# Kernel tuning notes

Hardware: AMD Instinct MI355X
Metric: run time of the kernel (lower is better)

## Reference

```python
import jax, jax.numpy as jnp
import numpy as np

B, S, H, NH = 4, 2048, 1024, 16
HD = H // NH
EPS = 1e-12


def setup_inputs() -> dict:
    key = jax.random.key(0)
    ks = jax.random.split(key, 12)
    sc = 0.02
    return {
        "query": jax.random.normal(ks[0], (B, S, H), dtype=jnp.float32),
        "attention_mask": jnp.zeros((B, 1, 1, S), dtype=jnp.float32),
        "Wq": jax.random.normal(ks[1], (H, H), dtype=jnp.float32) * sc,
        "bq": jnp.zeros((H,), dtype=jnp.float32),
        "Wk": jax.random.normal(ks[2], (H, H), dtype=jnp.float32) * sc,
        "bk": jnp.zeros((H,), dtype=jnp.float32),
        "Wv": jax.random.normal(ks[3], (H, H), dtype=jnp.float32) * sc,
        "bv": jnp.zeros((H,), dtype=jnp.float32),
        "Wd": jax.random.normal(ks[4], (H, H), dtype=jnp.float32) * sc,
        "bd": jnp.zeros((H,), dtype=jnp.float32),
        "ln_gamma": jnp.ones((H,), dtype=jnp.float32),
        "ln_beta": jnp.zeros((H,), dtype=jnp.float32),
    }


def reference(query, attention_mask, Wq, bq, Wk, bk, Wv, bv, Wd, bd, ln_gamma, ln_beta):
    # QKV projections: [B,S,H] -> [B,S,NH,HD]
    q = (query @ Wq + bq).reshape(B, S, NH, HD)
    k = (query @ Wk + bk).reshape(B, S, NH, HD)
    v = (query @ Wv + bv).reshape(B, S, NH, HD)
    # scores: [B,NH,S,S]
    scores = jnp.einsum("bqhd,bkhd->bhqk", q, k) / jnp.sqrt(jnp.float32(HD))
    scores = scores + attention_mask
    probs = jax.nn.softmax(scores, axis=-1)  # attn_dropout p=0 (eval)
    ctx = jnp.einsum("bhqk,bkhd->bqhd", probs, v).reshape(B, S, H)
    hidden = ctx @ Wd + bd  # out_dropout p=0 (eval)
    # pre-LN residual path: LN(hidden) + query
    mu = jnp.mean(hidden, axis=-1, keepdims=True)
    var = jnp.mean(jnp.square(hidden - mu), axis=-1, keepdims=True)
    hidden = (hidden - mu) * jax.lax.rsqrt(var + EPS) * ln_gamma + ln_beta
    return hidden + query
```

## Files before the change

### kernel.cpp

```cpp
#include <hip/hip_runtime.h>
#include <stdint.h>

#define Bn 4
#define Sn 2048
#define Hn 1024
#define NHn 16
#define Mn 8192

typedef unsigned short bf_t;
typedef __attribute__((ext_vector_type(8))) short s16x8;
typedef __attribute__((ext_vector_type(4))) short s16x4;
typedef __attribute__((ext_vector_type(8))) unsigned short u16x8;
typedef __attribute__((ext_vector_type(4))) unsigned short u16x4;
typedef __attribute__((ext_vector_type(4))) float f32x4;
typedef __attribute__((ext_vector_type(4))) unsigned int u32x4;
typedef __attribute__((ext_vector_type(2))) unsigned int u32x2;

__device__ __forceinline__ bf_t f2bf(float f) {
  unsigned int u = __float_as_uint(f);
  u += 0x7fffu + ((u >> 16) & 1u);
  return (bf_t)(u >> 16);
}

__device__ __forceinline__ unsigned pk2(float lo, float hi) {
  return __builtin_amdgcn_perm(__float_as_uint(hi), __float_as_uint(lo), 0x07060302u);
}
__device__ __forceinline__ s16x4 pack4(float a0, float a1, float a2, float a3) {
  u32x2 t;
  t[0] = pk2(a0, a1);
  t[1] = pk2(a2, a3);
  return __builtin_bit_cast(s16x4, t);
}

#define MFMA16K16(a, b, c) __builtin_amdgcn_mfma_f32_16x16x16bf16_1k(a, b, c, 0, 0, 0)

#define GLOAD16(gp, lp) __builtin_amdgcn_global_load_lds(              \
    (__attribute__((address_space(1))) void*)(gp),                     \
    (__attribute__((address_space(3))) void*)(lp), 16, 0, 0)

__global__ __launch_bounds__(256)
void cvt_bf16(const float* __restrict__ x, bf_t* __restrict__ y) {
  size_t i = ((size_t)blockIdx.x * 256 + threadIdx.x) * 4;
  const f32x4 v = *(const f32x4*)(x + i);
  u16x4 o;
  o[0] = f2bf(v[0]); o[1] = f2bf(v[1]); o[2] = f2bf(v[2]); o[3] = f2bf(v[3]);
  *(u16x4*)(y + i) = o;
}

__global__ __launch_bounds__(256)
void wtrans4(const float* __restrict__ Wq, const float* __restrict__ Wk,
             const float* __restrict__ Wv, const float* __restrict__ Wd,
             bf_t* __restrict__ Wt, bf_t* __restrict__ Wdt) {
  __shared__ float tile[32][33];
  const int z = blockIdx.z;
  const float* W = (z == 0) ? Wq : (z == 1) ? Wk : (z == 2) ? Wv : Wd;
  bf_t* dst = (z < 3) ? Wt + (size_t)z * Hn * Hn : Wdt;
  const int tx = threadIdx.x;
  const int ty = threadIdx.y;
  const int n0 = blockIdx.x * 32, k0 = blockIdx.y * 32;
#pragma unroll
  for (int i = 0; i < 4; i++)
    tile[ty + i * 8][tx] = W[(size_t)(k0 + ty + i * 8) * Hn + n0 + tx];
  __syncthreads();
#pragma unroll
  for (int i = 0; i < 4; i++) {
    const int nn = ty + i * 8, kk = tx;
    dst[(size_t)(n0 + nn) * Hn + k0 + kk] = f2bf(tile[kk][nn]);
  }
}

__global__ __launch_bounds__(256, 3)
void gemm_bt(const bf_t* __restrict__ A, const bf_t* __restrict__ Bt,
             const float* __restrict__ b0, const float* __restrict__ b1,
             const float* __restrict__ b2, void* __restrict__ outp,
             int N, int K, int out_bf16)
{
  __shared__ bf_t As[2][4096];
  __shared__ bf_t Bs[2][4096];
  const int tid = threadIdx.x;
  const int wave = tid >> 6, lane = tid & 63;
  const int l15 = lane & 15, quad = lane >> 4;
  const int bm = blockIdx.y * 128, bn = blockIdx.x * 128;
  const int wm = (wave >> 1) * 64, wn = (wave & 1) * 64;
  const int srow = tid >> 2;
  const int scol = (tid & 3) * 8;

  const bf_t* Ag = A + (size_t)(bm + srow) * K + scol;
  const bf_t* Bg = Bt + (size_t)(bn + srow) * K + scol;

  f32x4 acc[4][4] = {};

  GLOAD16(Ag, As[0] + tid * 8);
  GLOAD16(Ag + (size_t)64 * K, As[0] + 2048 + tid * 8);
  GLOAD16(Bg, Bs[0] + tid * 8);
  GLOAD16(Bg + (size_t)64 * K, Bs[0] + 2048 + tid * 8);

  const int nIter = K >> 5;
  for (int i = 0; i < nIter; i++) {
    const int cur = i & 1;
    __syncthreads();
    if (i + 1 < nIter) {
      const int k0 = (i + 1) * 32;
      GLOAD16(Ag + k0, As[cur ^ 1] + tid * 8);
      GLOAD16(Ag + (size_t)64 * K + k0, As[cur ^ 1] + 2048 + tid * 8);
      GLOAD16(Bg + k0, Bs[cur ^ 1] + tid * 8);
      GLOAD16(Bg + (size_t)64 * K + k0, Bs[cur ^ 1] + 2048 + tid * 8);
    }
    s16x8 af[4], bfr[4];
#pragma unroll
    for (int mi = 0; mi < 4; mi++)
      af[mi] = *(const s16x8*)&As[cur][(wm + mi * 16 + l15) * 32 + quad * 8];
#pragma unroll
    for (int ni = 0; ni < 4; ni++)
      bfr[ni] = *(const s16x8*)&Bs[cur][(wn + ni * 16 + l15) * 32 + quad * 8];
#pragma unroll
    for (int mi = 0; mi < 4; mi++)
#pragma unroll
      for (int ni = 0; ni < 4; ni++)
        acc[mi][ni] = __builtin_amdgcn_mfma_f32_16x16x32_bf16(af[mi], bfr[ni], acc[mi][ni], 0, 0, 0);
  }

#pragma unroll
  for (int ni = 0; ni < 4; ni++) {
    const int gn = bn + wn + ni * 16 + l15;
    const float* bp = (gn < 1024) ? b0 : ((gn < 2048) ? b1 : b2);
    const float bias = bp[gn & 1023];
#pragma unroll
    for (int mi = 0; mi < 4; mi++) {
#pragma unroll
      for (int r = 0; r < 4; r++) {
        const int gm = bm + wm + mi * 16 + quad * 4 + r;
        const float v = acc[mi][ni][r] + bias;
        if (out_bf16) ((bf_t*)outp)[(size_t)gm * N + gn] = f2bf(v);
        else          ((float*)outp)[(size_t)gm * N + gn] = v;
      }
    }
  }
}

__global__ __launch_bounds__(256)
void kvswz(const bf_t* __restrict__ qkv, bf_t* __restrict__ Kf,
           bf_t* __restrict__ Vf, const float* __restrict__ mask,
           float* __restrict__ mask2) {
  __shared__ u32x4 smbuf[640];
  const int t = threadIdx.x;
  const int bh = blockIdx.y, b = bh >> 4, h = bh & 15;
  const int k0 = blockIdx.x * 64;

  if (blockIdx.z == 0) {
    bf_t* KT = (bf_t*)smbuf;
#pragma unroll
    for (int i = 0; i < 2; i++) {
      const int c = t + i * 256;
      const int row = c >> 3, col8 = (c & 7) * 8;
      const u16x8 v = *(const u16x8*)(qkv + (size_t)(b * Sn + k0 + row) * 3072 + 1024 + h * 64 + col8);
      *(u16x8*)&KT[row * 80 + col8] = v;
    }
    __syncthreads();
    bf_t* dst0 = Kf + ((size_t)(bh * 32 + blockIdx.x) * 8) * 512;
#pragma unroll
    for (int i = 0; i < 2; i++) {
      const int p = t + i * 256;
      const int frag = p >> 6, lane = p & 63;
      const int ks = frag >> 1, half = frag & 1;
      const int l15 = lane & 15, quad = lane >> 4;
      const u16x8 v = *(const u16x8*)&KT[(ks * 16 + l15) * 80 + half * 32 + quad * 8];
      *(u16x8*)(dst0 + (size_t)frag * 512 + lane * 8) = v;
    }
  } else {
    unsigned int* P32 = (unsigned int*)smbuf;
    {
      const int kp = t >> 3;
      const int d0 = (t & 7) * 8;
      const bf_t* p0 = qkv + (size_t)(b * Sn + k0 + 2 * kp) * 3072 + 2048 + h * 64 + d0;
      const u16x8 r0 = *(const u16x8*)p0;
      const u16x8 r1 = *(const u16x8*)(p0 + 3072);
#pragma unroll
      for (int j = 0; j < 8; j++)
        P32[(d0 + j) * 33 + kp] = (unsigned)r0[j] | ((unsigned)r1[j] << 16);
    }
    if (h == 0 && t < 64)
      mask2[b * Sn + k0 + t] = mask[b * Sn + k0 + t] * 1.44269504f;
    __syncthreads();
    bf_t* dst0 = Vf + ((size_t)(bh * 32 + blockIdx.x) * 8) * 512;
#pragma unroll
    for (int i = 0; i < 2; i++) {
      const int p = t + i * 256;
      const int fp = p >> 6, lane = p & 63;
      const int dvblk = fp >> 1, kpair = fp & 1;
      const int l15 = lane & 15, quad = (lane >> 4) & 3;
      const int d = dvblk * 16 + l15;
      const int c = kpair * 16 + quad * 2;
      u32x4 w;
      w[0] = P32[d * 33 + c];
      w[1] = P32[d * 33 + c + 1];
      w[2] = P32[d * 33 + c + 8];
      w[3] = P32[d * 33 + c + 9];
      *(u32x4*)(dst0 + (size_t)fp * 512 + lane * 8) = w;
    }
  }
}

__global__ __launch_bounds__(256)
void attn(const bf_t* __restrict__ qkv, const bf_t* __restrict__ Kf,
          const bf_t* __restrict__ Vf, const float* __restrict__ mask2,
          bf_t* __restrict__ ctx)
{
  __shared__ bf_t Ks[2][4096];
  __shared__ bf_t Vs[2][4096];

  const int tid = threadIdx.x;
  const int wave = tid >> 6, lane = tid & 63;
  const int l15 = lane & 15, quad = lane >> 4;
  const int idx = blockIdx.x;
  const int bh = idx & 63, b = bh >> 4, h = bh & 15;
  const int q0 = (idx >> 6) * 128;

  s16x8 aq[2][2];
#pragma unroll
  for (int qf = 0; qf < 2; qf++) {
    const bf_t* qp = qkv + (size_t)(b * Sn + q0 + wave * 32 + qf * 16 + l15) * 3072 + h * 64;
    aq[qf][0] = *(const s16x8*)(qp + quad * 8);
    aq[qf][1] = *(const s16x8*)(qp + 32 + quad * 8);
  }

  f32x4 lacc[2] = {};
  f32x4 o[2][4] = {};
  const s16x4 ONES = {16256, 16256, 16256, 16256};

  const bf_t* kb = Kf + (size_t)bh * 32 * 4096;
  const bf_t* vb = Vf + (size_t)bh * 32 * 4096;
  const float* m2row = mask2 + (size_t)b * Sn;

  const float C1 = 0.125f * 1.44269504f;

#pragma unroll
  for (int c = 0; c < 2; c++) {
    GLOAD16(kb + c * 2048 + tid * 8, Ks[0] + c * 2048 + tid * 8);
    GLOAD16(vb + c * 2048 + tid * 8, Vs[0] + c * 2048 + tid * 8);
  }

  for (int it = 0; it < 32; ++it) {
    const int cur = it & 1;
    __syncthreads();
    if (it < 31) {
      const bf_t* kn = kb + (size_t)(it + 1) * 4096;
      const bf_t* vn = vb + (size_t)(it + 1) * 4096;
#pragma unroll
      for (int c = 0; c < 2; c++) {
        GLOAD16(kn + c * 2048 + tid * 8, Ks[cur ^ 1] + c * 2048 + tid * 8);
        GLOAD16(vn + c * 2048 + tid * 8, Vs[cur ^ 1] + c * 2048 + tid * 8);
      }
    }

    s16x4 pb[2][4];
#pragma unroll
    for (int e = 0; e < 4; e++) {
      const s16x8 k0f = *(const s16x8*)&Ks[cur][(e * 2 + 0) * 512 + lane * 8];
      const s16x8 k1f = *(const s16x8*)&Ks[cur][(e * 2 + 1) * 512 + lane * 8];
      const f32x4 mk2 = *(const f32x4*)(m2row + it * 64 + e * 16 + quad * 4);
#pragma unroll
      for (int qf = 0; qf < 2; qf++) {
        f32x4 acc = {};
        acc = __builtin_amdgcn_mfma_f32_16x16x32_bf16(k0f, aq[qf][0], acc, 0, 0, 0);
        acc = __builtin_amdgcn_mfma_f32_16x16x32_bf16(k1f, aq[qf][1], acc, 0, 0, 0);
        const float p0 = __builtin_exp2f(fmaf(acc[0], C1, mk2[0]));
        const float p1 = __builtin_exp2f(fmaf(acc[1], C1, mk2[1]));
        const float p2 = __builtin_exp2f(fmaf(acc[2], C1, mk2[2]));
        const float p3 = __builtin_exp2f(fmaf(acc[3], C1, mk2[3]));
        pb[qf][e] = pack4(p0, p1, p2, p3);
        lacc[qf] = MFMA16K16(ONES, pb[qf][e], lacc[qf]);
      }
    }

#pragma unroll
    for (int kpair = 0; kpair < 2; kpair++)
#pragma unroll
      for (int dvblk = 0; dvblk < 4; dvblk++) {
        const s16x8 vv = *(const s16x8*)&Vs[cur][(dvblk * 2 + kpair) * 512 + lane * 8];
        const s16x4 vlo = {vv[0], vv[1], vv[2], vv[3]};
        const s16x4 vhi = {vv[4], vv[5], vv[6], vv[7]};
#pragma unroll
        for (int qf = 0; qf < 2; qf++) {
          o[qf][dvblk] = MFMA16K16(vlo, pb[qf][kpair * 2 + 0], o[qf][dvblk]);
          o[qf][dvblk] = MFMA16K16(vhi, pb[qf][kpair * 2 + 1], o[qf][dvblk]);
        }
      }
  }

#pragma unroll
  for (int qf = 0; qf < 2; qf++) {
    const float inv = 1.f / lacc[qf][0];
    const size_t row = (size_t)(b * Sn + q0 + wave * 32 + qf * 16 + l15);
#pragma unroll
    for (int dvblk = 0; dvblk < 4; dvblk++) {
      u16x4 ov;
#pragma unroll
      for (int r = 0; r < 4; r++) ov[r] = f2bf(o[qf][dvblk][r] * inv);
      *(u16x4*)&ctx[row * Hn + h * 64 + dvblk * 16 + quad * 4] = ov;
    }
  }
}

__global__ __launch_bounds__(256)
void ln_res(const float* __restrict__ hid, const float* __restrict__ query,
            const float* __restrict__ gamma, const float* __restrict__ beta,
            float* __restrict__ out)
{
  const int row = blockIdx.x, t = threadIdx.x;
  const f32x4 h = *(const f32x4*)(hid + (size_t)row * Hn + t * 4);
  float s = h[0] + h[1] + h[2] + h[3];
  float ss = h[0]*h[0] + h[1]*h[1] + h[2]*h[2] + h[3]*h[3];
#pragma unroll
  for (int m = 32; m; m >>= 1) { s += __shfl_xor(s, m); ss += __shfl_xor(ss, m); }
  __shared__ float red[8];
  if ((t & 63) == 0) { red[t >> 6] = s; red[4 + (t >> 6)] = ss; }
  __syncthreads();
  s = red[0] + red[1] + red[2] + red[3];
  ss = red[4] + red[5] + red[6] + red[7];
  const float mu = s * (1.f / Hn);
  const float rs = rsqrtf(ss * (1.f / Hn) - mu * mu + 1e-12f);
  const f32x4 q = *(const f32x4*)(query + (size_t)row * Hn + t * 4);
  const f32x4 g = *(const f32x4*)(gamma + t * 4);
  const f32x4 be = *(const f32x4*)(beta + t * 4);
  f32x4 o;
#pragma unroll
  for (int j = 0; j < 4; j++) o[j] = (h[j] - mu) * rs * g[j] + be[j] + q[j];
  *(f32x4*)(out + (size_t)row * Hn + t * 4) = o;
}

extern "C" void kernel_launch(void* const* d_in, const int* in_sizes, int n_in,
                              void* d_out, int out_size, void* d_ws, size_t ws_size,
                              hipStream_t stream) {
  const float* query = (const float*)d_in[0];
  const float* mask  = (const float*)d_in[1];
  const float* Wq = (const float*)d_in[2];
  const float* bq = (const float*)d_in[3];
  const float* Wk = (const float*)d_in[4];
  const float* bk = (const float*)d_in[5];
  const float* Wv = (const float*)d_in[6];
  const float* bv = (const float*)d_in[7];
  const float* Wd = (const float*)d_in[8];
  const float* bd = (const float*)d_in[9];
  const float* gamma = (const float*)d_in[10];
  const float* beta  = (const float*)d_in[11];

  char* w = (char*)d_ws;
  bf_t* Xb  = (bf_t*)w;  w += (size_t)Mn * Hn * 2;
  bf_t* Wt  = (bf_t*)w;  w += (size_t)3 * Hn * Hn * 2;
  bf_t* Wdt = (bf_t*)w;  w += (size_t)Hn * Hn * 2;
  bf_t* QKV = (bf_t*)w;  w += (size_t)Mn * 3 * Hn * 2;
  bf_t* Vf  = (bf_t*)w;  w += (size_t)64 * 32 * 4096 * 2;
  bf_t* Ctx = (bf_t*)w;  w += (size_t)Mn * Hn * 2;
  bf_t* Kf  = (bf_t*)w;
  float* Hid = (float*)w;  w += (size_t)Mn * Hn * 4;
  float* Mask2 = (float*)w;

  cvt_bf16<<<Mn * Hn / 1024, 256, 0, stream>>>(query, Xb);
  wtrans4<<<dim3(32, 32, 4), dim3(32, 8), 0, stream>>>(Wq, Wk, Wv, Wd, Wt, Wdt);
  gemm_bt<<<dim3(24, 64), 256, 0, stream>>>(Xb, Wt, bq, bk, bv, QKV, 3072, 1024, 1);
  kvswz<<<dim3(32, 64, 2), 256, 0, stream>>>(QKV, Kf, Vf, mask, Mask2);
  attn<<<1024, 256, 0, stream>>>(QKV, Kf, Vf, Mask2, Ctx);
  gemm_bt<<<dim3(8, 64), 256, 0, stream>>>(Ctx, Wdt, bd, bd, bd, Hid, 1024, 1024, 0);
  ln_res<<<Mn, 256, 0, stream>>>(Hid, query, gamma, beta, (float*)d_out);
}
```

Baseline: 362.7 us.

## Merge prep kernels, stage mask in LDS, use native exp2 in attention

Combines the query-to-bf16 conversion and the weight transposes into one launch by adding a fifth z-slice that converts the query, which removes one kernel launch. The attention kernel now copies the 2048-entry mask row into shared memory once per block instead of reading it from global memory on every iteration. It also swaps exp2f for the native amdgcn exp2 intrinsic, which drops the range handling. The mask staging adds 8 KB of LDS per block, which may lower occupancy.

```diff
diff --git a/kernel.cpp b/kernel.cpp
--- a/kernel.cpp
+++ b/kernel.cpp
@@ -39,24 +39,29 @@
     (__attribute__((address_space(3))) void*)(lp), 16, 0, 0)
 
 __global__ __launch_bounds__(256)
-void cvt_bf16(const float* __restrict__ x, bf_t* __restrict__ y) {
-  size_t i = ((size_t)blockIdx.x * 256 + threadIdx.x) * 4;
-  const f32x4 v = *(const f32x4*)(x + i);
-  u16x4 o;
-  o[0] = f2bf(v[0]); o[1] = f2bf(v[1]); o[2] = f2bf(v[2]); o[3] = f2bf(v[3]);
-  *(u16x4*)(y + i) = o;
-}
-
-__global__ __launch_bounds__(256)
-void wtrans4(const float* __restrict__ Wq, const float* __restrict__ Wk,
-             const float* __restrict__ Wv, const float* __restrict__ Wd,
-             bf_t* __restrict__ Wt, bf_t* __restrict__ Wdt) {
+void prep(const float* __restrict__ Wq, const float* __restrict__ Wk,
+          const float* __restrict__ Wv, const float* __restrict__ Wd,
+          const float* __restrict__ query,
+          bf_t* __restrict__ Wt, bf_t* __restrict__ Wdt, bf_t* __restrict__ Xb) {
   __shared__ float tile[32][33];
   const int z = blockIdx.z;
+  const int tx = threadIdx.x;
+  const int ty = threadIdx.y;
+  if (z == 4) {
+    const int bid = blockIdx.y * 32 + blockIdx.x;
+    const int t = ty * 32 + tx;
+    const size_t base = (size_t)bid * 8192 + t * 4;
+#pragma unroll
+    for (int i = 0; i < 8; i++) {
+      const f32x4 v = *(const f32x4*)(query + base + i * 1024);
+      u16x4 o;
+      o[0] = f2bf(v[0]); o[1] = f2bf(v[1]); o[2] = f2bf(v[2]); o[3] = f2bf(v[3]);
+      *(u16x4*)(Xb + base + i * 1024) = o;
+    }
+    return;
+  }
   const float* W = (z == 0) ? Wq : (z == 1) ? Wk : (z == 2) ? Wv : Wd;
   bf_t* dst = (z < 3) ? Wt + (size_t)z * Hn * Hn : Wdt;
-  const int tx = threadIdx.x;
-  const int ty = threadIdx.y;
   const int n0 = blockIdx.x * 32, k0 = blockIdx.y * 32;
 #pragma unroll
   for (int i = 0; i < 4; i++)
@@ -208,6 +213,7 @@
 {
   __shared__ bf_t Ks[2][4096];
   __shared__ bf_t Vs[2][4096];
+  __shared__ float Ms[2048];
 
   const int tid = threadIdx.x;
   const int wave = tid >> 6, lane = tid & 63;
@@ -216,6 +222,14 @@
   const int bh = idx & 63, b = bh >> 4, h = bh & 15;
   const int q0 = (idx >> 6) * 128;
 
+  {
+    const float* m2row = mask2 + (size_t)b * Sn;
+    const f32x4 m0 = *(const f32x4*)(m2row + tid * 8);
+    const f32x4 m1 = *(const f32x4*)(m2row + tid * 8 + 4);
+    *(f32x4*)&Ms[tid * 8] = m0;
+    *(f32x4*)&Ms[tid * 8 + 4] = m1;
+  }
+
   s16x8 aq[2][2];
 #pragma unroll
   for (int qf = 0; qf < 2; qf++) {
@@ -230,7 +244,6 @@
 
   const bf_t* kb = Kf + (size_t)bh * 32 * 4096;
   const bf_t* vb = Vf + (size_t)bh * 32 * 4096;
-  const float* m2row = mask2 + (size_t)b * Sn;
 
   const float C1 = 0.125f * 1.44269504f;
 
@@ -258,16 +271,16 @@
     for (int e = 0; e < 4; e++) {
       const s16x8 k0f = *(const s16x8*)&Ks[cur][(e * 2 + 0) * 512 + lane * 8];
       const s16x8 k1f = *(const s16x8*)&Ks[cur][(e * 2 + 1) * 512 + lane * 8];
-      const f32x4 mk2 = *(const f32x4*)(m2row + it * 64 + e * 16 + quad * 4);
+      const f32x4 mk2 = *(const f32x4*)&Ms[it * 64 + e * 16 + quad * 4];
 #pragma unroll
       for (int qf = 0; qf < 2; qf++) {
         f32x4 acc = {};
         acc = __builtin_amdgcn_mfma_f32_16x16x32_bf16(k0f, aq[qf][0], acc, 0, 0, 0);
         acc = __builtin_amdgcn_mfma_f32_16x16x32_bf16(k1f, aq[qf][1], acc, 0, 0, 0);
-        const float p0 = __builtin_exp2f(fmaf(acc[0], C1, mk2[0]));
-        const float p1 = __builtin_exp2f(fmaf(acc[1], C1, mk2[1]));
-        const float p2 = __builtin_exp2f(fmaf(acc[2], C1, mk2[2]));
-        const float p3 = __builtin_exp2f(fmaf(acc[3], C1, mk2[3]));
+        const float p0 = __builtin_amdgcn_exp2f(fmaf(acc[0], C1, mk2[0]));
+        const float p1 = __builtin_amdgcn_exp2f(fmaf(acc[1], C1, mk2[1]));
+        const float p2 = __builtin_amdgcn_exp2f(fmaf(acc[2], C1, mk2[2]));
+        const float p3 = __builtin_amdgcn_exp2f(fmaf(acc[3], C1, mk2[3]));
         pb[qf][e] = pack4(p0, p1, p2, p3);
         lacc[qf] = MFMA16K16(ONES, pb[qf][e], lacc[qf]);
       }
@@ -356,8 +369,7 @@
   float* Hid = (float*)w;  w += (size_t)Mn * Hn * 4;
   float* Mask2 = (float*)w;
 
-  cvt_bf16<<<Mn * Hn / 1024, 256, 0, stream>>>(query, Xb);
-  wtrans4<<<dim3(32, 32, 4), dim3(32, 8), 0, stream>>>(Wq, Wk, Wv, Wd, Wt, Wdt);
+  prep<<<dim3(32, 32, 5), dim3(32, 8), 0, stream>>>(Wq, Wk, Wv, Wd, query, Wt, Wdt, Xb);
   gemm_bt<<<dim3(24, 64), 256, 0, stream>>>(Xb, Wt, bq, bk, bv, QKV, 3072, 1024, 1);
   kvswz<<<dim3(32, 64, 2), 256, 0, stream>>>(QKV, Kf, Vf, mask, Mask2);
   attn<<<1024, 256, 0, stream>>>(QKV, Kf, Vf, Mask2, Ctx);
```

Measured after the change: 333.8 us. 8.0% less time.
